# Performance work log

Hardware: AMD Instinct MI355X
Metric: run time of the kernel (lower is better)

Reference implementation:

```python
import jax, jax.numpy as jnp
import numpy as np

B, V, J, P = 1024, 5023, 5, 36
PARENTS = np.array([0, 0, 1, 1, 1], dtype=np.int64)  # FLAME kinematic chain


def setup_inputs() -> dict:
    key = jax.random.key(0)
    ks = jax.random.split(key, 8)
    return {
        "v_shaped_expressed": jax.random.normal(ks[0], (B, V, 3), jnp.float32) * 0.1,
        "global_pose_params_6d": jax.random.normal(ks[1], (B, 6), jnp.float32),
        "neck_pose_params_ax": jax.random.normal(ks[2], (B, 3), jnp.float32) * 0.1,
        "jaw_pose_params_ax": jax.random.normal(ks[3], (B, 3), jnp.float32) * 0.1,
        "eye_pose_params_ax": jax.random.normal(ks[4], (B, 6), jnp.float32) * 0.1,
        "J_transformed_rest": jax.random.normal(ks[5], (B, J, 3), jnp.float32) * 0.1,
        "lbs_weights": jax.nn.softmax(jax.random.normal(ks[6], (V, J), jnp.float32), axis=-1),
        "posedirs": jax.random.normal(ks[7], (V, P, 3), jnp.float32) * 0.01,
        "parents": jnp.asarray(PARENTS),
    }


def batch_rodrigues(rv, eps=1e-8):
    # rv: [B,3] axis-angle -> [B,3,3] rotation matrices
    angle = jnp.linalg.norm(rv + eps, axis=1, keepdims=True)  # [B,1]
    d = rv / angle
    cos = jnp.cos(angle)[:, :, None]
    sin = jnp.sin(angle)[:, :, None]
    rx, ry, rz = d[:, 0], d[:, 1], d[:, 2]
    z = jnp.zeros_like(rx)
    K = jnp.stack([z, -rz, ry, rz, z, -rx, -ry, rx, z], axis=1).reshape(-1, 3, 3)
    I = jnp.eye(3, dtype=rv.dtype)[None]
    return I + sin * K + (1.0 - cos) * (K @ K)


def rot6d_to_matrix(x):
    # Zhou et al. 6D rotation -> [B,3,3] (rows b1,b2,b3, as pytorch3d)
    a1, a2 = x[:, :3], x[:, 3:]
    b1 = a1 / jnp.linalg.norm(a1, axis=-1, keepdims=True)
    b2 = a2 - jnp.sum(b1 * a2, axis=-1, keepdims=True) * b1
    b2 = b2 / jnp.linalg.norm(b2, axis=-1, keepdims=True)
    b3 = jnp.cross(b1, b2)
    return jnp.stack([b1, b2, b3], axis=-2)


def make_T(R, t):
    # R [...,3,3], t [...,3] -> homogeneous [...,4,4]
    top = jnp.concatenate([R, t[..., None]], axis=-1)
    bot = jnp.broadcast_to(jnp.array([0.0, 0.0, 0.0, 1.0], R.dtype), top.shape[:-2] + (1, 4))
    return jnp.concatenate([top, bot], axis=-2)


def batch_rigid_transform(rot_mats, joints, parents):
    # rot_mats [B,J,3,3], joints [B,J,3]; parents: numpy int array (constant)
    rel = joints.at[:, 1:].add(-joints[:, parents[1:]])
    Tm = make_T(rot_mats, rel)  # [B,J,4,4]
    chain = [Tm[:, 0]]
    for i in range(1, parents.shape[0]):  # tiny fixed chain (J=5)
        chain.append(chain[int(parents[i])] @ Tm[:, i])
    tr = jnp.stack(chain, axis=1)  # [B,J,4,4]
    posed_joints = tr[:, :, :3, 3]
    R = tr[:, :, :3, :3]
    t = posed_joints - jnp.einsum('bjhw,bjw->bjh', R, joints)
    return posed_joints, make_T(R, t)


def reference(v_shaped_expressed, global_pose_params_6d, neck_pose_params_ax,
              jaw_pose_params_ax, eye_pose_params_ax, J_transformed_rest,
              lbs_weights, posedirs, parents):
    parents = np.asarray(parents)
    Rg = rot6d_to_matrix(global_pose_params_6d)
    Rn = batch_rodrigues(neck_pose_params_ax)
    Rj = batch_rodrigues(jaw_pose_params_ax)
    Rel = batch_rodrigues(eye_pose_params_ax[:, :3])
    Rer = batch_rodrigues(eye_pose_params_ax[:, 3:])
    rot_mats = jnp.stack([Rg, Rn, Rj, Rel, Rer], axis=1)  # [B,5,3,3]

    _, A = batch_rigid_transform(rot_mats, J_transformed_rest, parents)  # [B,5,4,4]

    # pose blendshapes from joints 1..4 (neck/jaw/eyes): [B, 36]
    b = rot_mats.shape[0]
    pose_feat = (rot_mats[:, 1:5] - jnp.eye(3, dtype=rot_mats.dtype)).reshape(b, -1)
    pose_bs = jnp.einsum('bp,vpc->bvc', pose_feat, posedirs)
    v = v_shaped_expressed + pose_bs  # [B,V,3]

    # linear blend skinning
    T = jnp.einsum('vj,bjhw->bvhw', lbs_weights, A)  # [B,V,4,4]
    v_h = jnp.concatenate([v, jnp.ones(v.shape[:2] + (1,), v.dtype)], axis=-1)
    v_posed = jnp.einsum('bvhw,bvw->bvh', T, v_h)[:, :, :3]
    return v_posed
```

## Files before the change

### kernel.cpp

```cpp
#include <hip/hip_runtime.h>
#include <math.h>

constexpr int Bn = 1024, Vn = 5023;
constexpr int NB = 16;
constexpr int PARAM_STRIDE = 96;

#define PIN(x) asm volatile("" : "+v"(x))


__device__ inline void rodrigues3(float rx, float ry, float rz, float R[9]) {
    const float eps = 1e-8f;
    float ax = rx + eps, ay = ry + eps, az = rz + eps;
    float ang = sqrtf(ax * ax + ay * ay + az * az);
    float inv = 1.0f / ang;
    float dx = rx * inv, dy = ry * inv, dz = rz * inv;
    float s = sinf(ang), c = cosf(ang), omc = 1.0f - c;
    float K[9] = {0.f, -dz, dy, dz, 0.f, -dx, -dy, dx, 0.f};
    float K2[9];
#pragma unroll
    for (int r = 0; r < 3; r++)
#pragma unroll
        for (int k = 0; k < 3; k++) {
            float acc = 0.f;
#pragma unroll
            for (int i = 0; i < 3; i++) acc += K[r * 3 + i] * K[i * 3 + k];
            K2[r * 3 + k] = acc;
        }
#pragma unroll
    for (int i = 0; i < 9; i++) R[i] = s * K[i] + omc * K2[i];
    R[0] += 1.f; R[4] += 1.f; R[8] += 1.f;
}

__device__ inline void rot6d(const float* x, float R[9]) {
    float a1x = x[0], a1y = x[1], a1z = x[2];
    float a2x = x[3], a2y = x[4], a2z = x[5];
    float n1 = sqrtf(a1x * a1x + a1y * a1y + a1z * a1z);
    float b1x = a1x / n1, b1y = a1y / n1, b1z = a1z / n1;
    float d = b1x * a2x + b1y * a2y + b1z * a2z;
    float tx = a2x - d * b1x, ty = a2y - d * b1y, tz = a2z - d * b1z;
    float n2 = sqrtf(tx * tx + ty * ty + tz * tz);
    float b2x = tx / n2, b2y = ty / n2, b2z = tz / n2;
    float b3x = b1y * b2z - b1z * b2y;
    float b3y = b1z * b2x - b1x * b2z;
    float b3z = b1x * b2y - b1y * b2x;
    R[0] = b1x; R[1] = b1y; R[2] = b1z;
    R[3] = b2x; R[4] = b2y; R[5] = b2z;
    R[6] = b3x; R[7] = b3y; R[8] = b3z;
}

__device__ inline void compose(const float* Rp, const float* tp,
                               const float* Ri, const float* ti,
                               float* Ro, float* to) {
#pragma unroll
    for (int r = 0; r < 3; r++) {
#pragma unroll
        for (int c = 0; c < 3; c++) {
            Ro[r * 3 + c] = Rp[r * 3 + 0] * Ri[0 * 3 + c] +
                            Rp[r * 3 + 1] * Ri[1 * 3 + c] +
                            Rp[r * 3 + 2] * Ri[2 * 3 + c];
        }
        to[r] = Rp[r * 3 + 0] * ti[0] + Rp[r * 3 + 1] * ti[1] +
                Rp[r * 3 + 2] * ti[2] + tp[r];
    }
}

__global__ void flame_params_kernel(const float* __restrict__ g6,
                                    const float* __restrict__ neck,
                                    const float* __restrict__ jaw,
                                    const float* __restrict__ eye,
                                    const float* __restrict__ jrest,
                                    float* __restrict__ params) {
    int b = blockIdx.x * blockDim.x + threadIdx.x;
    if (b >= Bn) return;

    float R[5][9];
    rot6d(g6 + b * 6, R[0]);
    rodrigues3(neck[b * 3 + 0], neck[b * 3 + 1], neck[b * 3 + 2], R[1]);
    rodrigues3(jaw[b * 3 + 0], jaw[b * 3 + 1], jaw[b * 3 + 2], R[2]);
    rodrigues3(eye[b * 6 + 0], eye[b * 6 + 1], eye[b * 6 + 2], R[3]);
    rodrigues3(eye[b * 6 + 3], eye[b * 6 + 4], eye[b * 6 + 5], R[4]);

    float j[5][3];
#pragma unroll
    for (int i = 0; i < 5; i++) {
        j[i][0] = jrest[b * 15 + i * 3 + 0];
        j[i][1] = jrest[b * 15 + i * 3 + 1];
        j[i][2] = jrest[b * 15 + i * 3 + 2];
    }
    float rel[5][3];
#pragma unroll
    for (int c = 0; c < 3; c++) {
        rel[0][c] = j[0][c];
        rel[1][c] = j[1][c] - j[0][c];
        rel[2][c] = j[2][c] - j[1][c];
        rel[3][c] = j[3][c] - j[1][c];
        rel[4][c] = j[4][c] - j[1][c];
    }

    float CR[5][9], CT[5][3];
#pragma unroll
    for (int i = 0; i < 9; i++) CR[0][i] = R[0][i];
#pragma unroll
    for (int c = 0; c < 3; c++) CT[0][c] = rel[0][c];
    compose(CR[0], CT[0], R[1], rel[1], CR[1], CT[1]);
    compose(CR[1], CT[1], R[2], rel[2], CR[2], CT[2]);
    compose(CR[1], CT[1], R[3], rel[3], CR[3], CT[3]);
    compose(CR[1], CT[1], R[4], rel[4], CR[4], CT[4]);

    float* P = params + b * PARAM_STRIDE;
#pragma unroll
    for (int jj = 0; jj < 4; jj++)
#pragma unroll
        for (int r = 0; r < 3; r++)
#pragma unroll
            for (int c = 0; c < 3; c++)
                P[jj * 9 + r * 3 + c] = R[jj + 1][r * 3 + c] - (r == c ? 1.f : 0.f);
#pragma unroll
    for (int i = 0; i < 5; i++) {
#pragma unroll
        for (int r = 0; r < 3; r++) {
            float t = CT[i][r] - (CR[i][r * 3 + 0] * j[i][0] +
                                  CR[i][r * 3 + 1] * j[i][1] +
                                  CR[i][r * 3 + 2] * j[i][2]);
            P[36 + i * 12 + r * 4 + 0] = CR[i][r * 3 + 0];
            P[36 + i * 12 + r * 4 + 1] = CR[i][r * 3 + 1];
            P[36 + i * 12 + r * 4 + 2] = CR[i][r * 3 + 2];
            P[36 + i * 12 + r * 4 + 3] = t;
        }
    }
}

__global__ __launch_bounds__(256, 3) void flame_main_kernel(
    const float* __restrict__ vsh, const float* __restrict__ lbs,
    const float* __restrict__ pdirs, const float* __restrict__ params,
    float* __restrict__ out) {
    int v = blockIdx.x * 256 + threadIdx.x;
    bool valid = v < Vn;
    int vc = valid ? v : (Vn - 1);
    int b0 = blockIdx.y * NB;

    const float* __restrict__ pv = pdirs + (size_t)vc * 108;
    float pd[108];
#pragma unroll
    for (int i = 0; i < 27; i++) {
        float4 t = *reinterpret_cast<const float4*>(pv + i * 4);
        pd[i * 4 + 0] = t.x;
        pd[i * 4 + 1] = t.y;
        pd[i * 4 + 2] = t.z;
        pd[i * 4 + 3] = t.w;
    }
#pragma unroll
    for (int i = 0; i < 108; i++) PIN(pd[i]);

    float w[5];
#pragma unroll
    for (int jj = 0; jj < 5; jj++) w[jj] = lbs[(size_t)vc * 5 + jj];

#pragma unroll 2
    for (int bi = 0; bi < NB; bi++) {
        int b = b0 + bi;
        const float4* __restrict__ P4 =
            reinterpret_cast<const float4*>(params + (size_t)b * PARAM_STRIDE);
        size_t base = ((size_t)b * Vn + vc) * 3;

        float3 vs = *reinterpret_cast<const float3*>(vsh + base);

        float px = 0.f, py = 0.f, pz = 0.f;
#pragma unroll
        for (int g = 0; g < 9; g++) {
            float4 f = P4[g];
            px = fmaf(f.x, pd[g * 12 + 0], px);
            py = fmaf(f.x, pd[g * 12 + 1], py);
            pz = fmaf(f.x, pd[g * 12 + 2], pz);
            px = fmaf(f.y, pd[g * 12 + 3], px);
            py = fmaf(f.y, pd[g * 12 + 4], py);
            pz = fmaf(f.y, pd[g * 12 + 5], pz);
            px = fmaf(f.z, pd[g * 12 + 6], px);
            py = fmaf(f.z, pd[g * 12 + 7], py);
            pz = fmaf(f.z, pd[g * 12 + 8], pz);
            px = fmaf(f.w, pd[g * 12 + 9], px);
            py = fmaf(f.w, pd[g * 12 + 10], py);
            pz = fmaf(f.w, pd[g * 12 + 11], pz);
        }

        float x = vs.x + px, y = vs.y + py, z = vs.z + pz;

        float ox = 0.f, oy = 0.f, oz = 0.f;
#pragma unroll
        for (int jj = 0; jj < 5; jj++) {
            float4 r0 = P4[9 + jj * 3 + 0];
            float4 r1 = P4[9 + jj * 3 + 1];
            float4 r2 = P4[9 + jj * 3 + 2];
            float wj = w[jj];
            float rx = fmaf(r0.x, x, fmaf(r0.y, y, fmaf(r0.z, z, r0.w)));
            float ry = fmaf(r1.x, x, fmaf(r1.y, y, fmaf(r1.z, z, r1.w)));
            float rz = fmaf(r2.x, x, fmaf(r2.y, y, fmaf(r2.z, z, r2.w)));
            ox = fmaf(wj, rx, ox);
            oy = fmaf(wj, ry, oy);
            oz = fmaf(wj, rz, oz);
        }
        if (valid) {
            float3 o;
            o.x = ox; o.y = oy; o.z = oz;
            *reinterpret_cast<float3*>(out + base) = o;
        }
    }
}

extern "C" void kernel_launch(void* const* d_in, const int* in_sizes, int n_in,
                              void* d_out, int out_size, void* d_ws, size_t ws_size,
                              hipStream_t stream) {
    const float* vsh   = (const float*)d_in[0];
    const float* g6    = (const float*)d_in[1];
    const float* neck  = (const float*)d_in[2];
    const float* jaw   = (const float*)d_in[3];
    const float* eye   = (const float*)d_in[4];
    const float* jrest = (const float*)d_in[5];
    const float* lbs   = (const float*)d_in[6];
    const float* pdirs = (const float*)d_in[7];
    float* out = (float*)d_out;
    float* params = (float*)d_ws;

    hipLaunchKernelGGL(flame_params_kernel, dim3((Bn + 255) / 256), dim3(256), 0,
                       stream, g6, neck, jaw, eye, jrest, params);

    dim3 grid((Vn + 255) / 256, Bn / NB);
    hipLaunchKernelGGL(flame_main_kernel, grid, dim3(256), 0, stream, vsh, lbs,
                       pdirs, params, out);
}
```

Measured before the change: 55.25 us.

## Split pose blendshape into three posedirs phases with per-batch accumulators

Restructures the main kernel so posedirs is loaded in three 36-float phases instead of holding all 108 values in registers. Each phase updates NB per-batch accumulators that start from the loaded v_shaped values, then the skinning loop runs over the batches. This is meant to cut peak register pressure from the 108-element array, at the cost of 48 live accumulators and reading the params rows for every batch three times. All vsh loads are now issued up front rather than interleaved with the compute.

```diff
diff --git a/kernel.cpp b/kernel.cpp
--- a/kernel.cpp
+++ b/kernel.cpp
@@ -130,6 +130,59 @@
     }
 }
 
+
+#define FMA3(FC, Q0, Q1, Q2)            \
+    ax[bi] = fmaf(FC, Q0, ax[bi]);      \
+    ay[bi] = fmaf(FC, Q1, ay[bi]);      \
+    az[bi] = fmaf(FC, Q2, az[bi]);
+
+#define POSE_PHASE(PH)                                                         \
+    {                                                                          \
+        float4 t0 = *reinterpret_cast<const float4*>(pv + PH * 36 + 0);        \
+        float4 t1 = *reinterpret_cast<const float4*>(pv + PH * 36 + 4);        \
+        float4 t2 = *reinterpret_cast<const float4*>(pv + PH * 36 + 8);        \
+        float4 t3 = *reinterpret_cast<const float4*>(pv + PH * 36 + 12);       \
+        float4 t4 = *reinterpret_cast<const float4*>(pv + PH * 36 + 16);       \
+        float4 t5 = *reinterpret_cast<const float4*>(pv + PH * 36 + 20);       \
+        float4 t6 = *reinterpret_cast<const float4*>(pv + PH * 36 + 24);       \
+        float4 t7 = *reinterpret_cast<const float4*>(pv + PH * 36 + 28);       \
+        float4 t8 = *reinterpret_cast<const float4*>(pv + PH * 36 + 32);       \
+        float q0 = t0.x, q1 = t0.y, q2 = t0.z, q3 = t0.w;                      \
+        float q4 = t1.x, q5 = t1.y, q6 = t1.z, q7 = t1.w;                      \
+        float q8 = t2.x, q9 = t2.y, q10 = t2.z, q11 = t2.w;                    \
+        float q12 = t3.x, q13 = t3.y, q14 = t3.z, q15 = t3.w;                  \
+        float q16 = t4.x, q17 = t4.y, q18 = t4.z, q19 = t4.w;                  \
+        float q20 = t5.x, q21 = t5.y, q22 = t5.z, q23 = t5.w;                  \
+        float q24 = t6.x, q25 = t6.y, q26 = t6.z, q27 = t6.w;                  \
+        float q28 = t7.x, q29 = t7.y, q30 = t7.z, q31 = t7.w;                  \
+        float q32 = t8.x, q33 = t8.y, q34 = t8.z, q35 = t8.w;                  \
+        PIN(q0); PIN(q1); PIN(q2); PIN(q3); PIN(q4); PIN(q5);                  \
+        PIN(q6); PIN(q7); PIN(q8); PIN(q9); PIN(q10); PIN(q11);                \
+        PIN(q12); PIN(q13); PIN(q14); PIN(q15); PIN(q16); PIN(q17);            \
+        PIN(q18); PIN(q19); PIN(q20); PIN(q21); PIN(q22); PIN(q23);            \
+        PIN(q24); PIN(q25); PIN(q26); PIN(q27); PIN(q28); PIN(q29);            \
+        PIN(q30); PIN(q31); PIN(q32); PIN(q33); PIN(q34); PIN(q35);            \
+        _Pragma("unroll") for (int bi = 0; bi < NB; bi++) {                    \
+            const float4* P4 = reinterpret_cast<const float4*>(                \
+                params + (size_t)(b0 + bi) * PARAM_STRIDE);                    \
+            float4 f0 = P4[PH * 3 + 0];                                        \
+            float4 f1 = P4[PH * 3 + 1];                                        \
+            float4 f2 = P4[PH * 3 + 2];                                        \
+            FMA3(f0.x, q0, q1, q2)                                             \
+            FMA3(f0.y, q3, q4, q5)                                             \
+            FMA3(f0.z, q6, q7, q8)                                             \
+            FMA3(f0.w, q9, q10, q11)                                           \
+            FMA3(f1.x, q12, q13, q14)                                          \
+            FMA3(f1.y, q15, q16, q17)                                          \
+            FMA3(f1.z, q18, q19, q20)                                          \
+            FMA3(f1.w, q21, q22, q23)                                          \
+            FMA3(f2.x, q24, q25, q26)                                          \
+            FMA3(f2.y, q27, q28, q29)                                          \
+            FMA3(f2.z, q30, q31, q32)                                          \
+            FMA3(f2.w, q33, q34, q35)                                          \
+        }                                                                      \
+    }
+
 __global__ __launch_bounds__(256, 3) void flame_main_kernel(
     const float* __restrict__ vsh, const float* __restrict__ lbs,
     const float* __restrict__ pdirs, const float* __restrict__ params,
@@ -140,57 +193,36 @@
     int b0 = blockIdx.y * NB;
 
     const float* __restrict__ pv = pdirs + (size_t)vc * 108;
-    float pd[108];
-#pragma unroll
-    for (int i = 0; i < 27; i++) {
-        float4 t = *reinterpret_cast<const float4*>(pv + i * 4);
-        pd[i * 4 + 0] = t.x;
-        pd[i * 4 + 1] = t.y;
-        pd[i * 4 + 2] = t.z;
-        pd[i * 4 + 3] = t.w;
-    }
-#pragma unroll
-    for (int i = 0; i < 108; i++) PIN(pd[i]);
+
+    float ax[NB], ay[NB], az[NB];
+#pragma unroll
+    for (int bi = 0; bi < NB; bi++) {
+        size_t base = ((size_t)(b0 + bi) * Vn + vc) * 3;
+        float3 vs = *reinterpret_cast<const float3*>(vsh + base);
+        ax[bi] = vs.x;
+        ay[bi] = vs.y;
+        az[bi] = vs.z;
+    }
 
     float w[5];
 #pragma unroll
     for (int jj = 0; jj < 5; jj++) w[jj] = lbs[(size_t)vc * 5 + jj];
 
-#pragma unroll 2
+    POSE_PHASE(0)
+    POSE_PHASE(1)
+    POSE_PHASE(2)
+
+#pragma unroll
     for (int bi = 0; bi < NB; bi++) {
-        int b = b0 + bi;
-        const float4* __restrict__ P4 =
-            reinterpret_cast<const float4*>(params + (size_t)b * PARAM_STRIDE);
-        size_t base = ((size_t)b * Vn + vc) * 3;
-
-        float3 vs = *reinterpret_cast<const float3*>(vsh + base);
-
-        float px = 0.f, py = 0.f, pz = 0.f;
-#pragma unroll
-        for (int g = 0; g < 9; g++) {
-            float4 f = P4[g];
-            px = fmaf(f.x, pd[g * 12 + 0], px);
-            py = fmaf(f.x, pd[g * 12 + 1], py);
-            pz = fmaf(f.x, pd[g * 12 + 2], pz);
-            px = fmaf(f.y, pd[g * 12 + 3], px);
-            py = fmaf(f.y, pd[g * 12 + 4], py);
-            pz = fmaf(f.y, pd[g * 12 + 5], pz);
-            px = fmaf(f.z, pd[g * 12 + 6], px);
-            py = fmaf(f.z, pd[g * 12 + 7], py);
-            pz = fmaf(f.z, pd[g * 12 + 8], pz);
-            px = fmaf(f.w, pd[g * 12 + 9], px);
-            py = fmaf(f.w, pd[g * 12 + 10], py);
-            pz = fmaf(f.w, pd[g * 12 + 11], pz);
-        }
-
-        float x = vs.x + px, y = vs.y + py, z = vs.z + pz;
-
+        const float4* __restrict__ A4 = reinterpret_cast<const float4*>(
+            params + (size_t)(b0 + bi) * PARAM_STRIDE + 36);
+        float x = ax[bi], y = ay[bi], z = az[bi];
         float ox = 0.f, oy = 0.f, oz = 0.f;
 #pragma unroll
         for (int jj = 0; jj < 5; jj++) {
-            float4 r0 = P4[9 + jj * 3 + 0];
-            float4 r1 = P4[9 + jj * 3 + 1];
-            float4 r2 = P4[9 + jj * 3 + 2];
+            float4 r0 = A4[jj * 3 + 0];
+            float4 r1 = A4[jj * 3 + 1];
+            float4 r2 = A4[jj * 3 + 2];
             float wj = w[jj];
             float rx = fmaf(r0.x, x, fmaf(r0.y, y, fmaf(r0.z, z, r0.w)));
             float ry = fmaf(r1.x, x, fmaf(r1.y, y, fmaf(r1.z, z, r1.w)));
@@ -200,6 +232,7 @@
             oz = fmaf(wj, rz, oz);
         }
         if (valid) {
+            size_t base = ((size_t)(b0 + bi) * Vn + vc) * 3;
             float3 o;
             o.x = ox; o.y = oy; o.z = oz;
             *reinterpret_cast<float3*>(out + base) = o;
```

New measurement: 77.36 us. +40.0%, slower.
